# Kernel optimization log

Hardware: AMD Instinct MI355X
Metric: run time of the kernel (lower is better)

Reference implementation:

```python
import jax, jax.numpy as jnp
import numpy as np

# DCNv4 config (matches init_kwargs)
C = 64; G = 4; GC = C // G          # group channels = 16
KS = 3; KP = KS * KS                # 9 sampling points per group
DIL = 1; OFFSET_SCALE = 1.0
OM_DIM = int(np.ceil(G * KP * 3 / 8) * 8)  # 112 (padded offset+mask dim)
N, H, W = 4, 128, 128


def setup_inputs() -> dict:
    key = jax.random.key(0)
    ks = jax.random.split(key, 5)
    x = jax.random.normal(ks[0], (N, C, H, W), dtype=jnp.float32)
    value_w = jax.random.normal(ks[1], (C, C), dtype=jnp.float32) * (1.0 / np.sqrt(C))
    value_b = jnp.zeros((C,), dtype=jnp.float32)
    # small random offset/mask projection (torch zero-init would be degenerate)
    om_w = jax.random.normal(ks[2], (OM_DIM, C), dtype=jnp.float32) * 0.02
    om_b = jax.random.normal(ks[3], (OM_DIM,), dtype=jnp.float32) * 0.02
    out_w = jax.random.normal(ks[4], (C, C), dtype=jnp.float32) * (1.0 / np.sqrt(C))
    out_b = jnp.zeros((C,), dtype=jnp.float32)
    return {"x": x, "value_w": value_w, "value_b": value_b,
            "om_w": om_w, "om_b": om_b, "out_w": out_w, "out_b": out_b}


def _dcnv4_core(v, off, mask, Hh, Ww):
    # v: (N, L, G, GC)   off: (N, L, G, KP, 2) (x,y)   mask: (N, L, G, KP)
    n, L = v.shape[0], v.shape[1]
    py = (jnp.arange(L) // Ww).astype(jnp.float32)          # (L,)
    px = (jnp.arange(L) % Ww).astype(jnp.float32)
    r = (KS - 1) // 2
    dy, dx = jnp.meshgrid(jnp.arange(-r, r + 1, dtype=jnp.float32) * DIL,
                          jnp.arange(-r, r + 1, dtype=jnp.float32) * DIL,
                          indexing="ij")
    dy = dy.reshape(-1); dx = dx.reshape(-1)                # (KP,)
    # sampling coords: (N, L, G, KP)
    sy = py[None, :, None, None] + dy[None, None, None, :] + off[..., 1] * OFFSET_SCALE
    sx = px[None, :, None, None] + dx[None, None, None, :] + off[..., 0] * OFFSET_SCALE

    y0 = jnp.floor(sy); x0 = jnp.floor(sx)
    wy = sy - y0; wx = sx - x0
    vg = v.transpose(0, 2, 1, 3)                            # (N, G, L, GC)

    def gather(yc, xc, wgt):
        valid = ((yc >= 0) & (yc < Hh) & (xc >= 0) & (xc < Ww)).astype(v.dtype)
        yi = jnp.clip(yc, 0, Hh - 1).astype(jnp.int32)
        xi = jnp.clip(xc, 0, Ww - 1).astype(jnp.int32)
        idx = (yi * Ww + xi).transpose(0, 2, 1, 3).reshape(n, G, L * KP)  # (N,G,L*KP)
        g = jnp.take_along_axis(vg, idx[..., None], axis=2)              # (N,G,L*KP,GC)
        w = (wgt * valid).transpose(0, 2, 1, 3).reshape(n, G, L * KP, 1)
        return g * w

    samp = (gather(y0, x0, (1 - wy) * (1 - wx))
            + gather(y0, x0 + 1, (1 - wy) * wx)
            + gather(y0 + 1, x0, wy * (1 - wx))
            + gather(y0 + 1, x0 + 1, wy * wx))               # (N,G,L*KP,GC)
    samp = samp.reshape(n, G, L, KP, GC)
    m = mask.transpose(0, 2, 1, 3)[..., None]                # (N,G,L,KP,1)
    out = (samp * m).sum(axis=3)                             # (N,G,L,GC)
    return out.transpose(0, 2, 1, 3).reshape(n, L, G * GC)


def reference(x, value_w, value_b, om_w, om_b, out_w, out_b):
    n, c, Hh, Ww = x.shape
    L = Hh * Ww
    inp = x.transpose(0, 2, 3, 1).reshape(n, L, c)           # (N, L, C)
    v = (inp @ value_w.T + value_b).reshape(n, L, G, GC)     # value_proj
    om = inp @ om_w.T + om_b                                 # (N, L, 112)
    om = om[..., :G * KP * 3].reshape(n, L, G, KP * 3)       # per-group [off(2K), mask(K)]
    off = om[..., :2 * KP].reshape(n, L, G, KP, 2)
    mask = om[..., 2 * KP:]                                  # no softmax in DCNv4
    y = _dcnv4_core(v, off, mask, Hh, Ww)                    # (N, L, C)
    y = y @ out_w.T + out_b                                  # output_proj
    return y.reshape(n, Hh, Ww, c).transpose(0, 3, 1, 2)     # (N, C, H, W)
```

## Files before the change

kernel.cpp:

```cpp
#include <hip/hip_runtime.h>

#define NN 4
#define CC 64
#define GG 4
#define GCC 16
#define HH 128
#define WW 128
#define LL (HH*WW)
#define OMS 112
#define WPC 192

__global__ void pack_kernel(const float* __restrict__ value_w, const float* __restrict__ value_b,
                            const float* __restrict__ om_w,    const float* __restrict__ om_b,
                            const float* __restrict__ out_w,
                            float* __restrict__ wpack, float* __restrict__ bpack,
                            float* __restrict__ owt)
{
  const int i = blockIdx.x * 256 + threadIdx.x;
  if (i < 64 * WPC) {
    const int k = i / WPC, c = i % WPC;
    float v = 0.0f;
    if (c < 64) v = value_w[c * 64 + k];
    else if (c < 176) {
      const int s = c - 64;
      if (s % 28 != 27) { const int r = s - s / 28; v = om_w[r * 64 + k]; }
    }
    wpack[i] = v;
  }
  if (i < WPC) {
    float v = 0.0f;
    if (i < 64) v = value_b[i];
    else if (i < 176) {
      const int s = i - 64;
      if (s % 28 != 27) { const int r = s - s / 28; v = om_b[r]; }
    }
    bpack[i] = v;
  }
  if (i < 64 * 64) {
    const int k = i >> 6, c = i & 63;
    owt[i] = out_w[c * 64 + k];
  }
}

__global__ __launch_bounds__(256) void vm_kernel(
    const float* __restrict__ x, const float* __restrict__ wpack,
    const float* __restrict__ bpack,
    float* __restrict__ vws, float* __restrict__ omws)
{
  __shared__ float wlds[64][16];
  const int t    = threadIdx.x;
  const int ch   = blockIdx.y;
  const int col0 = ch << 4;

  {
    const int k = t >> 2, q = t & 3;
    *(float4*)&wlds[k][q * 4] =
        *(const float4*)&wpack[k * WPC + col0 + q * 4];
  }
  float b[16];
  #pragma unroll
  for (int j = 0; j < 16; ++j) b[j] = bpack[col0 + j];
  __syncthreads();

  const int l0 = blockIdx.x << 10;
  const int n  = l0 >> 14;
  const int hw = (l0 & (LL - 1)) + t;

  float acc[4][16];
  #pragma unroll
  for (int pi = 0; pi < 4; ++pi)
    #pragma unroll
    for (int j = 0; j < 16; ++j) acc[pi][j] = b[j];

  const float* xb = x + (size_t)n * CC * LL + hw;
  #pragma unroll 8
  for (int k = 0; k < 64; ++k) {
    float xv[4];
    #pragma unroll
    for (int pi = 0; pi < 4; ++pi) xv[pi] = xb[(size_t)k * LL + pi * 256];
    #pragma unroll
    for (int q = 0; q < 4; ++q) {
      const float4 w = *(const float4*)&wlds[k][q * 4];
      #pragma unroll
      for (int pi = 0; pi < 4; ++pi) {
        acc[pi][q*4+0] = fmaf(xv[pi], w.x, acc[pi][q*4+0]);
        acc[pi][q*4+1] = fmaf(xv[pi], w.y, acc[pi][q*4+1]);
        acc[pi][q*4+2] = fmaf(xv[pi], w.z, acc[pi][q*4+2]);
        acc[pi][q*4+3] = fmaf(xv[pi], w.w, acc[pi][q*4+3]);
      }
    }
  }

  float* dst; int col; int stride;
  if (ch < 4) { dst = vws  + (size_t)n * LL * 64;  col = col0;      stride = 64;  }
  else        { dst = omws + (size_t)n * LL * OMS; col = col0 - 64; stride = OMS; }
  #pragma unroll
  for (int pi = 0; pi < 4; ++pi) {
    float* d = dst + (size_t)(hw + pi * 256) * stride + col;
    #pragma unroll
    for (int q = 0; q < 4; ++q)
      *(float4*)&d[q * 4] =
          make_float4(acc[pi][q*4+0], acc[pi][q*4+1], acc[pi][q*4+2], acc[pi][q*4+3]);
  }
}

__global__ __launch_bounds__(512) void dcn_kernel(
    const float* __restrict__ vws, const float* __restrict__ omws,
    const float* __restrict__ owt, const float* __restrict__ out_b,
    float* __restrict__ out)
{
  __shared__ float s_lds[128][68];
  __shared__ float owlds[64 * 64];
  const int t   = threadIdx.x;
  const int B   = blockIdx.x;
  const int xcd = B & 7;
  const int n   = xcd >> 1;
  const int row = ((xcd & 1) << 6) | (B >> 3);
  const int l0  = row << 7;

  {
    const float4* s4 = (const float4*)owt;
    float4*       d4 = (float4*)owlds;
    d4[t]       = s4[t];
    d4[512 + t] = s4[512 + t];
  }

  {
    const int p = t >> 2;
    const int g = t & 3;
    const int l = l0 + p;
    const float pyf = (float)row;
    const float pxf = (float)p;
    const float* __restrict__ omp_  = omws + ((size_t)n * LL + l) * OMS + g * 28;
    const float* __restrict__ vbase = vws + (size_t)n * LL * CC + g * GCC;

    float buf[28];
    const float4* og4 = (const float4*)omp_;
    #pragma unroll
    for (int i = 0; i < 7; ++i) {
      const float4 vv = og4[i];
      buf[4*i+0] = vv.x; buf[4*i+1] = vv.y; buf[4*i+2] = vv.z; buf[4*i+3] = vv.w;
    }

    float s[16];
    #pragma unroll
    for (int i = 0; i < 16; ++i) s[i] = 0.0f;

    #pragma unroll
    for (int pp = 0; pp < 9; ++pp) {
      const float sy  = pyf + (float)(pp / 3 - 1) + buf[2*pp+1];
      const float sx  = pxf + (float)(pp % 3 - 1) + buf[2*pp+0];
      const float y0f = floorf(sy), x0f = floorf(sx);
      const float wy  = sy - y0f,  wx  = sx - x0f;
      const int   iy  = (int)y0f,  ix  = (int)x0f;
      const float m   = buf[18 + pp];
      const float w00 = (1.0f - wy) * (1.0f - wx) * m;
      const float w01 = (1.0f - wy) * wx * m;
      const float w10 = wy * (1.0f - wx) * m;
      const float w11 = wy * wx * m;
      #pragma unroll
      for (int cor = 0; cor < 4; ++cor) {
        const int   cy = iy + (cor >> 1);
        const int   cx = ix + (cor & 1);
        const float w  = (cor == 0) ? w00 : (cor == 1) ? w01 : (cor == 2) ? w10 : w11;
        if (cy >= 0 && cy < HH && cx >= 0 && cx < WW) {
          const float4* vp4 = (const float4*)(vbase + (size_t)(cy * WW + cx) * CC);
          #pragma unroll
          for (int qq = 0; qq < 4; ++qq) {
            const float4 vv = vp4[qq];
            s[4*qq+0] = fmaf(w, vv.x, s[4*qq+0]);
            s[4*qq+1] = fmaf(w, vv.y, s[4*qq+1]);
            s[4*qq+2] = fmaf(w, vv.z, s[4*qq+2]);
            s[4*qq+3] = fmaf(w, vv.w, s[4*qq+3]);
          }
        }
      }
    }
    #pragma unroll
    for (int q = 0; q < 4; ++q)
      *(float4*)&s_lds[p][g * 16 + q * 4] =
          make_float4(s[4*q+0], s[4*q+1], s[4*q+2], s[4*q+3]);
  }
  __syncthreads();

  {
    const int w  = t >> 6;
    const int p  = (t & 63) | ((w & 1) << 6);
    const int cq = w >> 1;
    float y[16];
    #pragma unroll
    for (int j = 0; j < 16; ++j) y[j] = out_b[cq * 16 + j];
    #pragma unroll 4
    for (int k4 = 0; k4 < 16; ++k4) {
      const float4 sv = *(const float4*)&s_lds[p][k4 * 4];
      #pragma unroll
      for (int e = 0; e < 4; ++e) {
        const float se = (e == 0) ? sv.x : (e == 1) ? sv.y : (e == 2) ? sv.z : sv.w;
        const int   k  = k4 * 4 + e;
        #pragma unroll
        for (int q = 0; q < 4; ++q) {
          const float4 wv = *(const float4*)&owlds[k * 64 + cq * 16 + q * 4];
          y[q*4+0] = fmaf(se, wv.x, y[q*4+0]);
          y[q*4+1] = fmaf(se, wv.y, y[q*4+1]);
          y[q*4+2] = fmaf(se, wv.z, y[q*4+2]);
          y[q*4+3] = fmaf(se, wv.w, y[q*4+3]);
        }
      }
    }
    float* op = out + ((size_t)n * CC) * LL + l0 + p;
    #pragma unroll
    for (int j = 0; j < 16; ++j)
      op[(size_t)(cq * 16 + j) * LL] = y[j];
  }
}

extern "C" void kernel_launch(void* const* d_in, const int* in_sizes, int n_in,
                              void* d_out, int out_size, void* d_ws, size_t ws_size,
                              hipStream_t stream) {
  const float* x       = (const float*)d_in[0];
  const float* value_w = (const float*)d_in[1];
  const float* value_b = (const float*)d_in[2];
  const float* om_w    = (const float*)d_in[3];
  const float* om_b    = (const float*)d_in[4];
  const float* out_w   = (const float*)d_in[5];
  const float* out_b   = (const float*)d_in[6];
  float* outp = (float*)d_out;

  float* vws   = (float*)d_ws;
  float* omws  = vws   + (size_t)NN * LL * CC;
  float* wpack = omws  + (size_t)NN * LL * OMS;
  float* bpack = wpack + 64 * WPC;
  float* owt   = bpack + WPC;

  pack_kernel<<<dim3(48), dim3(256), 0, stream>>>(
      value_w, value_b, om_w, om_b, out_w, wpack, bpack, owt);
  vm_kernel<<<dim3(64, 11), dim3(256), 0, stream>>>(
      x, wpack, bpack, vws, omws);
  dcn_kernel<<<dim3(512), dim3(512), 0, stream>>>(
      vws, omws, owt, out_b, outp);
}
```

Before: 161.0 us.

## Split DCN sampling across 4 threads per group and quarter-row blocks

The DCN kernel now assigns each (pixel, group) to four threads, each handling one float4 of channels, so every block covers 32 pixels instead of 128 and the grid grows to 2048 blocks. The output projection is likewise split so that each thread produces 4 output channels instead of 16. The aim is more parallelism and fewer registers per thread, which should hide the latency of the gather loads. The cost is that every thread now redundantly loads the offsets and recomputes the bilinear weights, blocks reload the out-weight matrix four times as often, and output stores are only 32 pixels wide.

Result: faster. 151.1 us (-6.1%).

```diff
diff --git a/kernel.cpp b/kernel.cpp
--- a/kernel.cpp
+++ b/kernel.cpp
@@ -109,14 +109,15 @@
     const float* __restrict__ owt, const float* __restrict__ out_b,
     float* __restrict__ out)
 {
-  __shared__ float s_lds[128][68];
+  __shared__ float s_lds[32][68];
   __shared__ float owlds[64 * 64];
   const int t   = threadIdx.x;
   const int B   = blockIdx.x;
   const int xcd = B & 7;
   const int n   = xcd >> 1;
-  const int row = ((xcd & 1) << 6) | (B >> 3);
-  const int l0  = row << 7;
+  const int idx = ((xcd & 1) << 8) | (B >> 3);
+  const int row = idx >> 2;
+  const int l0  = (row << 7) + ((idx & 3) << 5);
 
   {
     const float4* s4 = (const float4*)owt;
@@ -126,13 +127,14 @@
   }
 
   {
-    const int p = t >> 2;
-    const int g = t & 3;
-    const int l = l0 + p;
+    const int px = t >> 4;
+    const int g  = (t >> 2) & 3;
+    const int qq = t & 3;
+    const int l  = l0 + px;
     const float pyf = (float)row;
-    const float pxf = (float)p;
+    const float pxf = (float)(l & (WW - 1));
     const float* __restrict__ omp_  = omws + ((size_t)n * LL + l) * OMS + g * 28;
-    const float* __restrict__ vbase = vws + (size_t)n * LL * CC + g * GCC;
+    const float* __restrict__ vbase = vws + (size_t)n * LL * CC + g * GCC + qq * 4;
 
     float buf[28];
     const float4* og4 = (const float4*)omp_;
@@ -142,9 +144,7 @@
       buf[4*i+0] = vv.x; buf[4*i+1] = vv.y; buf[4*i+2] = vv.z; buf[4*i+3] = vv.w;
     }
 
-    float s[16];
-    #pragma unroll
-    for (int i = 0; i < 16; ++i) s[i] = 0.0f;
+    float s0 = 0.0f, s1 = 0.0f, s2 = 0.0f, s3 = 0.0f;
 
     #pragma unroll
     for (int pp = 0; pp < 9; ++pp) {
@@ -164,53 +164,42 @@
         const int   cx = ix + (cor & 1);
         const float w  = (cor == 0) ? w00 : (cor == 1) ? w01 : (cor == 2) ? w10 : w11;
         if (cy >= 0 && cy < HH && cx >= 0 && cx < WW) {
-          const float4* vp4 = (const float4*)(vbase + (size_t)(cy * WW + cx) * CC);
-          #pragma unroll
-          for (int qq = 0; qq < 4; ++qq) {
-            const float4 vv = vp4[qq];
-            s[4*qq+0] = fmaf(w, vv.x, s[4*qq+0]);
-            s[4*qq+1] = fmaf(w, vv.y, s[4*qq+1]);
-            s[4*qq+2] = fmaf(w, vv.z, s[4*qq+2]);
-            s[4*qq+3] = fmaf(w, vv.w, s[4*qq+3]);
-          }
+          const float4 vv = *(const float4*)(vbase + (size_t)(cy * WW + cx) * CC);
+          s0 = fmaf(w, vv.x, s0);
+          s1 = fmaf(w, vv.y, s1);
+          s2 = fmaf(w, vv.z, s2);
+          s3 = fmaf(w, vv.w, s3);
         }
       }
     }
-    #pragma unroll
-    for (int q = 0; q < 4; ++q)
-      *(float4*)&s_lds[p][g * 16 + q * 4] =
-          make_float4(s[4*q+0], s[4*q+1], s[4*q+2], s[4*q+3]);
+    *(float4*)&s_lds[px][g * 16 + qq * 4] = make_float4(s0, s1, s2, s3);
   }
   __syncthreads();
 
   {
-    const int w  = t >> 6;
-    const int p  = (t & 63) | ((w & 1) << 6);
-    const int cq = w >> 1;
-    float y[16];
-    #pragma unroll
-    for (int j = 0; j < 16; ++j) y[j] = out_b[cq * 16 + j];
+    const int px = t & 31;
+    const int c4 = t >> 5;
+    const int l  = l0 + px;
+    float y0 = out_b[c4 * 4 + 0], y1 = out_b[c4 * 4 + 1];
+    float y2 = out_b[c4 * 4 + 2], y3 = out_b[c4 * 4 + 3];
     #pragma unroll 4
     for (int k4 = 0; k4 < 16; ++k4) {
-      const float4 sv = *(const float4*)&s_lds[p][k4 * 4];
+      const float4 sv = *(const float4*)&s_lds[px][k4 * 4];
       #pragma unroll
       for (int e = 0; e < 4; ++e) {
         const float se = (e == 0) ? sv.x : (e == 1) ? sv.y : (e == 2) ? sv.z : sv.w;
-        const int   k  = k4 * 4 + e;
-        #pragma unroll
-        for (int q = 0; q < 4; ++q) {
-          const float4 wv = *(const float4*)&owlds[k * 64 + cq * 16 + q * 4];
-          y[q*4+0] = fmaf(se, wv.x, y[q*4+0]);
-          y[q*4+1] = fmaf(se, wv.y, y[q*4+1]);
-          y[q*4+2] = fmaf(se, wv.z, y[q*4+2]);
-          y[q*4+3] = fmaf(se, wv.w, y[q*4+3]);
-        }
+        const float4 wv = *(const float4*)&owlds[(k4 * 4 + e) * 64 + c4 * 4];
+        y0 = fmaf(se, wv.x, y0);
+        y1 = fmaf(se, wv.y, y1);
+        y2 = fmaf(se, wv.z, y2);
+        y3 = fmaf(se, wv.w, y3);
       }
     }
-    float* op = out + ((size_t)n * CC) * LL + l0 + p;
-    #pragma unroll
-    for (int j = 0; j < 16; ++j)
-      op[(size_t)(cq * 16 + j) * LL] = y[j];
+    float* op = out + ((size_t)n * CC) * LL + l;
+    op[(size_t)(c4 * 4 + 0) * LL] = y0;
+    op[(size_t)(c4 * 4 + 1) * LL] = y1;
+    op[(size_t)(c4 * 4 + 2) * LL] = y2;
+    op[(size_t)(c4 * 4 + 3) * LL] = y3;
   }
 }
 
@@ -236,6 +225,6 @@
       value_w, value_b, om_w, om_b, out_w, wpack, bpack, owt);
   vm_kernel<<<dim3(64, 11), dim3(256), 0, stream>>>(
       x, wpack, bpack, vws, omws);
-  dcn_kernel<<<dim3(512), dim3(512), 0, stream>>>(
+  dcn_kernel<<<dim3(2048), dim3(512), 0, stream>>>(
       vws, omws, owt, out_b, outp);
 }
```
